# Kernel tuning notes

Hardware: AMD Instinct MI355X
Metric: run time of the kernel (lower is better)

The kernel has to match this reference:

```python
import jax, jax.numpy as jnp
import numpy as np

D_MODEL = 768
N_HEADS = 12
D_HEAD = 64
INIT_RANGE = 0.02
IGNORE = -100000.0


def setup_inputs() -> dict:
    key = jax.random.key(0)
    ks = jax.random.split(key, 5)
    x = jax.random.normal(ks[0], (2, 2048, D_MODEL), dtype=jnp.float32)
    W_Q = INIT_RANGE * jax.random.normal(ks[1], (N_HEADS, D_MODEL, D_HEAD), dtype=jnp.float32)
    W_K = INIT_RANGE * jax.random.normal(ks[2], (N_HEADS, D_MODEL, D_HEAD), dtype=jnp.float32)
    W_V = INIT_RANGE * jax.random.normal(ks[3], (N_HEADS, D_MODEL, D_HEAD), dtype=jnp.float32)
    W_O = INIT_RANGE * jax.random.normal(ks[4], (N_HEADS, D_HEAD, D_MODEL), dtype=jnp.float32)
    b_Q = jnp.zeros((N_HEADS, D_HEAD), dtype=jnp.float32)
    b_K = jnp.zeros((N_HEADS, D_HEAD), dtype=jnp.float32)
    b_V = jnp.zeros((N_HEADS, D_HEAD), dtype=jnp.float32)
    b_O = jnp.zeros((D_MODEL,), dtype=jnp.float32)
    return {"x": x, "W_Q": W_Q, "b_Q": b_Q, "W_K": W_K, "b_K": b_K,
            "W_V": W_V, "b_V": b_V, "W_O": W_O, "b_O": b_O}


def reference(x, W_Q, b_Q, W_K, b_K, W_V, b_V, W_O, b_O):
    # x: [b, s, m]; W_*: [h, m, d]
    Q = jnp.einsum('bsm,hmd->bshd', x, W_Q) + b_Q  # [b, s, h, d]
    K = jnp.einsum('bsm,hmd->bshd', x, W_K) + b_K
    V = jnp.einsum('bsm,hmd->bshd', x, W_V) + b_V
    scores = jnp.einsum('bqhd,bkhd->bhqk', Q, K) / jnp.sqrt(jnp.float32(D_HEAD))
    s = scores.shape[-1]
    causal = jnp.triu(jnp.ones((s, s), dtype=bool), k=1)  # True above diagonal
    scores = jnp.where(causal, jnp.float32(IGNORE), scores)
    pattern = jax.nn.softmax(scores, axis=-1)  # [b, h, q, k]
    Z = jnp.einsum('bhqk,bkhd->bqhd', pattern, V)
    out = jnp.einsum('bqhd,hdm->bqm', Z, W_O) + b_O
    return out
```

## Files before the change

kernel.cpp:

```cpp
#include <hip/hip_runtime.h>
#include <hip/hip_bf16.h>

#define BATCH 2
#define SLEN 2048
#define NH 12
#define DM 768
#define DH 64
#define ROWS (BATCH*SLEN)
#define NQKV (3*DM)
#define NCHUNK 51

typedef __attribute__((ext_vector_type(8))) short bf16x8;
typedef __attribute__((ext_vector_type(4))) float f32x4;
typedef unsigned short u16;
typedef unsigned int u32;
typedef __attribute__((ext_vector_type(4))) unsigned short u16x4;
typedef __attribute__((ext_vector_type(8))) unsigned short u16x8;

__device__ __forceinline__ u16 f2b(float f) {
    unsigned int u = __builtin_bit_cast(unsigned int, f);
    unsigned int r = (u + 0x7FFFu + ((u >> 16) & 1u)) >> 16;
    return (u16)r;
}
__device__ __forceinline__ float b2f(u16 v) {
    unsigned int u = ((unsigned int)v) << 16;
    return __builtin_bit_cast(float, u);
}

__device__ __forceinline__ void gload16(const u16* g, u16* l) {
    __builtin_amdgcn_global_load_lds(
        (const __attribute__((address_space(1))) unsigned int*)g,
        (__attribute__((address_space(3))) unsigned int*)l,
        16, 0, 0);
}


__global__ __launch_bounds__(256) void pack_x(const float* __restrict__ x, u16* __restrict__ xb) {
    int i = blockIdx.x * 256 + threadIdx.x;
    const float4* xv = (const float4*)x;
    float4 a = xv[i * 2], b = xv[i * 2 + 1];
    u16x8 o;
    o[0] = f2b(a.x); o[1] = f2b(a.y); o[2] = f2b(a.z); o[3] = f2b(a.w);
    o[4] = f2b(b.x); o[5] = f2b(b.y); o[6] = f2b(b.z); o[7] = f2b(b.w);
    *(u16x8*)(xb + (size_t)i * 8) = o;
}

__global__ __launch_bounds__(256) void pack_wqkv(const float* __restrict__ WQ, const float* __restrict__ WK,
                                                 const float* __restrict__ WV, u16* __restrict__ out) {
    __shared__ u16 L[64 * 72];
    int mt = blockIdx.x, h = blockIdx.y, sel = blockIdx.z;
    const float* W = sel == 0 ? WQ : (sel == 1 ? WK : WV);
    const float* src = W + ((size_t)h * DM + mt * 64) * DH;
    int t = threadIdx.x;
    for (int j = 0; j < 4; j++) {
        int i = t + 256 * j;
        int r = i >> 4, cf = i & 15;
        float4 v = ((const float4*)src)[i];
        u16x4 o; o[0] = f2b(v.x); o[1] = f2b(v.y); o[2] = f2b(v.z); o[3] = f2b(v.w);
        *(u16x4*)&L[r * 72 + cf * 4] = o;
    }
    __syncthreads();
    u16* orow = out + ((size_t)(sel * DM + h * DH)) * DM + mt * 64;
    for (int j = 0; j < 16; j++) {
        int e = t + 256 * j;
        int d = e >> 6, mm = e & 63;
        orow[(size_t)d * DM + mm] = L[mm * 72 + d];
    }
}

__global__ __launch_bounds__(256) void pack_wo(const float* __restrict__ WO, u16* __restrict__ out) {
    __shared__ u16 L[64 * 72];
    int bi = blockIdx.x, bj = blockIdx.y;
    int t = threadIdx.x;
    for (int j = 0; j < 4; j++) {
        int i = t + 256 * j;
        int r = i >> 4, cf = i & 15;
        float4 v = ((const float4*)(WO + (size_t)(bi * 64 + r) * DM + bj * 64))[cf];
        u16x4 o; o[0] = f2b(v.x); o[1] = f2b(v.y); o[2] = f2b(v.z); o[3] = f2b(v.w);
        *(u16x4*)&L[r * 72 + cf * 4] = o;
    }
    __syncthreads();
    for (int j = 0; j < 16; j++) {
        int e = t + 256 * j;
        int c = e >> 6, r = e & 63;
        out[(size_t)(bj * 64 + c) * DM + bi * 64 + r] = L[r * 72 + c];
    }
}


__global__ __launch_bounds__(256) void gemm_qkv(const u16* __restrict__ A, const u16* __restrict__ Bt,
                                                const float* __restrict__ bQ, const float* __restrict__ bK,
                                                const float* __restrict__ bV,
                                                u16* __restrict__ Qb, u16* __restrict__ Kb, u16* __restrict__ Vb) {
    __shared__ u16 Al[128 * 64];
    __shared__ u16 Bl[128 * 64];
    int t = threadIdx.x;
    int n0 = blockIdx.x * 128, m0 = blockIdx.y * 128;
    int lane = t & 63, w = t >> 6;
    int ln = lane & 15, qd = lane >> 4;
    int wr = (w & 1) * 64, wc = (w >> 1) * 64;
    int srow = lane >> 3, slot = lane & 7;
    f32x4 acc[4][4] = {};

    for (int kt = 0; kt < DM / 64; kt++) {
        __syncthreads();
        for (int j = 0; j < 4; j++) {
            int r = w * 32 + j * 8 + srow;
            int gc = slot ^ (r & 7);
            gload16(A + (size_t)(m0 + r) * DM + kt * 64 + gc * 8, &Al[(w * 32 + j * 8) * 64]);
            gload16(Bt + (size_t)(n0 + r) * DM + kt * 64 + gc * 8, &Bl[(w * 32 + j * 8) * 64]);
        }
        __syncthreads();
        for (int ks = 0; ks < 2; ks++) {
            int sl = ((ks * 4 + qd) ^ (ln & 7)) * 8;
            bf16x8 af[4], bfr[4];
            for (int rt = 0; rt < 4; rt++)
                af[rt] = *(const bf16x8*)&Al[(wr + rt * 16 + ln) * 64 + sl];
            for (int ct = 0; ct < 4; ct++)
                bfr[ct] = *(const bf16x8*)&Bl[(wc + ct * 16 + ln) * 64 + sl];
            for (int rt = 0; rt < 4; rt++)
                for (int ct = 0; ct < 4; ct++)
                    acc[rt][ct] = __builtin_amdgcn_mfma_f32_16x16x32_bf16(af[rt], bfr[ct], acc[rt][ct], 0, 0, 0);
        }
    }
    int sel = n0 / DM;
    if (sel == 2) {
        for (int ct = 0; ct < 4; ct++) {
            int col = n0 - 2 * DM + wc + ct * 16 + ln;
            int hh = col >> 6, dd = col & 63;
            float bv = bV[col];
            for (int rt = 0; rt < 4; rt++) {
                int row = m0 + wr + rt * 16 + qd * 4;
                int bb = row >> 11, ss = row & 2047;
                u16x4 pk;
                for (int r = 0; r < 4; r++) pk[r] = f2b(acc[rt][ct][r] + bv);
                *(u16x4*)&Vb[(((size_t)bb * NH + hh) * DH + dd) * SLEN + ss] = pk;
            }
        }
    } else {
        const float* bias = sel == 0 ? bQ : bK;
        u16* Out = sel == 0 ? Qb : Kb;
        const float qs = sel == 0 ? 0.125f * 1.44269504f : 1.0f;
        for (int ct = 0; ct < 4; ct++) {
            int col = n0 - sel * DM + wc + ct * 16 + ln;
            int hh = col >> 6, dd = col & 63;
            float bv = bias[col];
            for (int rt = 0; rt < 4; rt++) {
                int row = m0 + wr + rt * 16 + qd * 4;
                for (int r = 0; r < 4; r++) {
                    int rg = row + r;
                    int bb = rg >> 11, ss = rg & 2047;
                    Out[(((size_t)bb * NH + hh) * SLEN + ss) * DH + dd] = f2b((acc[rt][ct][r] + bv) * qs);
                }
            }
        }
    }
}


__device__ __forceinline__ void cid2qc(int cid, int& p, int& c, int& nc) {
    p = 0;
    int base = 0;
    while (true) {
        int n = p / 3 + 1;
        if (cid < base + n) { c = cid - base; nc = n; return; }
        base += n; p++;
    }
}

__global__ __launch_bounds__(256, 4) void attn(const u16* __restrict__ Qb, const u16* __restrict__ Kb,
                                               const u16* __restrict__ Vtg,
                                               u16* __restrict__ Po, float* __restrict__ Plv) {
    __shared__ u16 Kl[64 * 64];
    __shared__ u16 Vt[64 * 64];
    __shared__ u16 Pq[4 * 32 * 64];
    int cid = blockIdx.x, bh = blockIdx.y;
    int p, c, nc;
    cid2qc(cid, p, c, nc);
    int ntiles = 2 * p + 2;
    int kt0 = c * ntiles / nc, kt1 = (c + 1) * ntiles / nc;
    const u16* Qp = Qb + (size_t)bh * SLEN * DH;
    const u16* Kp = Kb + (size_t)bh * SLEN * DH;
    const u16* Vp = Vtg + (size_t)bh * SLEN * DH;
    int t = threadIdx.x, lane = t & 63, w = t >> 6;
    int ln = lane & 15, qd = lane >> 4;
    int srow = lane >> 3, slot = lane & 7;
    int qbA = p * 128 + w * 32, qbB = qbA + 16;

    bf16x8 qfA[2], qfB[2];
    for (int ks = 0; ks < 2; ks++) {
        qfA[ks] = *(const bf16x8*)(Qp + (size_t)(qbA + ln) * DH + ks * 32 + qd * 8);
        qfB[ks] = *(const bf16x8*)(Qp + (size_t)(qbB + ln) * DH + ks * 32 + qd * 8);
    }

    float lA = 0.f, lB = 0.f;
    f32x4 oA[4] = {}, oB[4] = {};

    u16* PwA = Pq + w * 32 * 64;
    u16* PwB = PwA + 16 * 64;

    for (int kt = kt0; kt < kt1; kt++) {
        int k0 = kt * 64;
        __syncthreads();
        for (int j = 0; j < 2; j++) {
            int r = w * 16 + j * 8 + srow;
            int gc = slot ^ (r & 7);
            gload16(Kp + (size_t)(k0 + r) * DH + gc * 8, &Kl[(w * 16 + j * 8) * 64]);
            gload16(Vp + (size_t)r * SLEN + k0 + gc * 8, &Vt[(w * 16 + j * 8) * 64]);
        }
        __syncthreads();

        f32x4 sfA[4] = {}, sfB[4] = {};
        for (int ks = 0; ks < 2; ks++) {
            int sl = ((ks * 4 + qd) ^ (ln & 7)) * 8;
            for (int ct = 0; ct < 4; ct++) {
                bf16x8 kf = *(const bf16x8*)&Kl[(ct * 16 + ln) * 64 + sl];
                sfA[ct] = __builtin_amdgcn_mfma_f32_16x16x32_bf16(kf, qfA[ks], sfA[ct], 0, 0, 0);
                sfB[ct] = __builtin_amdgcn_mfma_f32_16x16x32_bf16(kf, qfB[ks], sfB[ct], 0, 0, 0);
            }
        }

        if (kt >= (qbA >> 6)) {
            int qg = qbA + ln;
            for (int ct = 0; ct < 4; ct++)
                for (int r = 0; r < 4; r++) {
                    int kg = k0 + ct * 16 + qd * 4 + r;
                    if (kg > qg) sfA[ct][r] = -1e30f;
                }
        }
        if (kt >= (qbB >> 6)) {
            int qg = qbB + ln;
            for (int ct = 0; ct < 4; ct++)
                for (int r = 0; r < 4; r++) {
                    int kg = k0 + ct * 16 + qd * 4 + r;
                    if (kg > qg) sfB[ct][r] = -1e30f;
                }
        }

        float sA = 0.f, sB = 0.f;
        for (int ct = 0; ct < 4; ct++) {
            u32 ea[4], eb[4];
            for (int r = 0; r < 4; r++) {
                float eA = exp2f(sfA[ct][r]);
                float eB = exp2f(sfB[ct][r]);
                ea[r] = __builtin_bit_cast(u32, eA);
                eb[r] = __builtin_bit_cast(u32, eB);
                sA += __builtin_bit_cast(float, ea[r] & 0xFFFF0000u);
                sB += __builtin_bit_cast(float, eb[r] & 0xFFFF0000u);
            }
            uint2 pkA, pkB;
            pkA.x = __builtin_amdgcn_perm(ea[1], ea[0], 0x07060302u);
            pkA.y = __builtin_amdgcn_perm(ea[3], ea[2], 0x07060302u);
            pkB.x = __builtin_amdgcn_perm(eb[1], eb[0], 0x07060302u);
            pkB.y = __builtin_amdgcn_perm(eb[3], eb[2], 0x07060302u);
            int off = (((ct * 2 + (qd >> 1)) ^ (ln & 7)) * 8) + (qd & 1) * 4;
            *(uint2*)&PwA[ln * 64 + off] = pkA;
            *(uint2*)&PwB[ln * 64 + off] = pkB;
        }
        lA += sA; lB += sB;

        for (int ks = 0; ks < 2; ks++) {
            int sl = ((ks * 4 + qd) ^ (ln & 7)) * 8;
            bf16x8 pfA = *(const bf16x8*)&PwA[ln * 64 + sl];
            bf16x8 pfB = *(const bf16x8*)&PwB[ln * 64 + sl];
            for (int dt = 0; dt < 4; dt++) {
                bf16x8 vf = *(const bf16x8*)&Vt[(dt * 16 + ln) * 64 + sl];
                oA[dt] = __builtin_amdgcn_mfma_f32_16x16x32_bf16(vf, pfA, oA[dt], 0, 0, 0);
                oB[dt] = __builtin_amdgcn_mfma_f32_16x16x32_bf16(vf, pfB, oB[dt], 0, 0, 0);
            }
        }
    }

    lA += __shfl_xor(lA, 16, 64);
    lA += __shfl_xor(lA, 32, 64);
    lB += __shfl_xor(lB, 16, 64);
    lB += __shfl_xor(lB, 32, 64);

    size_t pid = (size_t)bh * NCHUNK + cid;
    u16* op = Po + pid * 8192;
    for (int dt = 0; dt < 4; dt++) {
        u16x4 ovA, ovB;
        for (int r = 0; r < 4; r++) { ovA[r] = f2b(oA[dt][r]); ovB[r] = f2b(oB[dt][r]); }
        *(u16x4*)&op[(w * 32 + ln) * 64 + dt * 16 + qd * 4] = ovA;
        *(u16x4*)&op[(w * 32 + 16 + ln) * 64 + dt * 16 + qd * 4] = ovB;
    }
    if (qd == 0) {
        Plv[pid * 128 + w * 32 + ln] = lA;
        Plv[pid * 128 + w * 32 + 16 + ln] = lB;
    }
}


__global__ __launch_bounds__(256) void combine(const u16* __restrict__ Po, const float* __restrict__ Plv,
                                               u16* __restrict__ Zb) {
    int p = blockIdx.x, bh = blockIdx.y;
    int b = bh / NH, h = bh % NH;
    int g = p / 3, i = p % 3;
    int nc = g + 1;
    int base = 3 * (g * (g + 1) / 2) + i * (g + 1);
    int t = threadIdx.x;
    int q = t >> 1, dseg = (t & 1) * 32;

    float acc[32] = {};
    float lsum = 0.f;
    for (int cc = 0; cc < nc; cc++) {
        size_t pid = (size_t)bh * NCHUNK + base + cc;
        lsum += Plv[pid * 128 + q];
        const u16* op = Po + pid * 8192 + q * 64 + dseg;
        for (int j = 0; j < 4; j++) {
            u16x8 v = *(const u16x8*)(op + j * 8);
            for (int e = 0; e < 8; e++)
                acc[j * 8 + e] += b2f(v[e]);
        }
    }
    float inv = 1.0f / lsum;
    u16* Zp = Zb + ((size_t)b * SLEN + p * 128 + q) * DM + h * DH + dseg;
    for (int j = 0; j < 4; j++) {
        u16x8 ov;
        for (int e = 0; e < 8; e++) ov[e] = f2b(acc[j * 8 + e] * inv);
        *(u16x8*)(Zp + j * 8) = ov;
    }
}


__global__ __launch_bounds__(256) void gemm_proj(const u16* __restrict__ A, const u16* __restrict__ Bt,
                                                 const float* __restrict__ bO, float* __restrict__ out) {
    __shared__ u16 Al[64 * 64];
    __shared__ u16 Bl[96 * 64];
    int t = threadIdx.x;
    int n0 = blockIdx.x * 96, m0 = blockIdx.y * 64;
    int lane = t & 63, w = t >> 6;
    int ln = lane & 15, qd = lane >> 4;
    int wr = (w & 1) * 32, wc = (w >> 1) * 48;
    int srow = lane >> 3, slot = lane & 7;
    f32x4 acc[2][3] = {};

    for (int kt = 0; kt < DM / 64; kt++) {
        __syncthreads();
        for (int j = 0; j < 2; j++) {
            int r = w * 16 + j * 8 + srow;
            int gc = slot ^ (r & 7);
            gload16(A + (size_t)(m0 + r) * DM + kt * 64 + gc * 8, &Al[(w * 16 + j * 8) * 64]);
        }
        for (int j = 0; j < 3; j++) {
            int r = w * 24 + j * 8 + srow;
            int gc = slot ^ (r & 7);
            gload16(Bt + (size_t)(n0 + r) * DM + kt * 64 + gc * 8, &Bl[(w * 24 + j * 8) * 64]);
        }
        __syncthreads();
        for (int ks = 0; ks < 2; ks++) {
            int sl = ((ks * 4 + qd) ^ (ln & 7)) * 8;
            bf16x8 af[2], bfr[3];
            for (int rt = 0; rt < 2; rt++)
                af[rt] = *(const bf16x8*)&Al[(wr + rt * 16 + ln) * 64 + sl];
            for (int ct = 0; ct < 3; ct++)
                bfr[ct] = *(const bf16x8*)&Bl[(wc + ct * 16 + ln) * 64 + sl];
            for (int rt = 0; rt < 2; rt++)
                for (int ct = 0; ct < 3; ct++)
                    acc[rt][ct] = __builtin_amdgcn_mfma_f32_16x16x32_bf16(af[rt], bfr[ct], acc[rt][ct], 0, 0, 0);
        }
    }
    for (int ct = 0; ct < 3; ct++) {
        int col = n0 + wc + ct * 16 + ln;
        float bv = bO[col];
        for (int rt = 0; rt < 2; rt++) {
            int row = m0 + wr + rt * 16 + qd * 4;
            for (int r = 0; r < 4; r++)
                out[(size_t)(row + r) * DM + col] = acc[rt][ct][r] + bv;
        }
    }
}


extern "C" void kernel_launch(void* const* d_in, const int* in_sizes, int n_in,
                              void* d_out, int out_size, void* d_ws, size_t ws_size,
                              hipStream_t stream) {
    const float* x  = (const float*)d_in[0];
    const float* WQ = (const float*)d_in[1];
    const float* bQ = (const float*)d_in[2];
    const float* WK = (const float*)d_in[3];
    const float* bK = (const float*)d_in[4];
    const float* WV = (const float*)d_in[5];
    const float* bV = (const float*)d_in[6];
    const float* WO = (const float*)d_in[7];
    const float* bO = (const float*)d_in[8];
    float* out = (float*)d_out;

    u16* xb   = (u16*)d_ws;
    u16* wqkv = xb + (size_t)ROWS * DM;
    u16* wo   = wqkv + (size_t)NQKV * DM;
    u16* Qb   = wo + (size_t)DM * DM;
    size_t hsz = (size_t)BATCH * NH * SLEN * DH;
    u16* Kb   = Qb + hsz;
    u16* Vb   = Kb + hsz;
    u16* Zb   = Vb + hsz;
    u16* Po   = Zb + (size_t)ROWS * DM;
    float* Pl = (float*)(Po + (size_t)BATCH * NH * NCHUNK * 8192);

    pack_x<<<ROWS * DM / 2048, 256, 0, stream>>>(x, xb);
    pack_wqkv<<<dim3(12, 12, 3), 256, 0, stream>>>(WQ, WK, WV, wqkv);
    pack_wo<<<dim3(12, 12), 256, 0, stream>>>(WO, wo);
    gemm_qkv<<<dim3(NQKV / 128, ROWS / 128), 256, 0, stream>>>(xb, wqkv, bQ, bK, bV, Qb, Kb, Vb);
    attn<<<dim3(NCHUNK, BATCH * NH), 256, 0, stream>>>(Qb, Kb, Vb, Po, Pl);
    combine<<<dim3(SLEN / 128, BATCH * NH), 256, 0, stream>>>(Po, Pl, Zb);
    gemm_proj<<<dim3(DM / 96, ROWS / 64), 256, 0, stream>>>(Zb, wo, bO, out);
}
```

Measured before the change: 182.8 us.

## Double-buffer K/V tiles in attention and remap grid to a 1D interleaved order

The attention kernel now keeps two LDS buffers for the K and V tiles. It issues the load of the next tile right after the barrier, so the global-to-LDS copy overlaps the current tile's QK and PV MFMAs, and each iteration needs one barrier instead of two. The per-wave P scratch shrinks to one 16x64 tile that the A and B query halves use in turn, which offsets part of the extra LDS from double buffering. The launch becomes a 1D grid that interleaves batch-head indices across consecutive blocks, likely to spread K/V reuse across XCDs and caches. Total LDS per block rises, which could limit occupancy, and reusing one P buffer serializes the two softmax/PV halves.

New measurement: 202.8 us. 10.9% more time.

```diff
diff --git a/kernel.cpp b/kernel.cpp
--- a/kernel.cpp
+++ b/kernel.cpp
@@ -171,10 +171,13 @@
 __global__ __launch_bounds__(256, 4) void attn(const u16* __restrict__ Qb, const u16* __restrict__ Kb,
                                                const u16* __restrict__ Vtg,
                                                u16* __restrict__ Po, float* __restrict__ Plv) {
-    __shared__ u16 Kl[64 * 64];
-    __shared__ u16 Vt[64 * 64];
-    __shared__ u16 Pq[4 * 32 * 64];
-    int cid = blockIdx.x, bh = blockIdx.y;
+    __shared__ u16 Kl[2][64 * 64];
+    __shared__ u16 Vt[2][64 * 64];
+    __shared__ u16 Pq[4][16 * 64];
+    int blk = blockIdx.x;
+    int j24 = blk % 24;
+    int cid = blk / 24;
+    int bh = (j24 & 7) * 3 + (j24 >> 3);
     int p, c, nc;
     cid2qc(cid, p, c, nc);
     int ntiles = 2 * p + 2;
@@ -195,26 +198,57 @@
 
     float lA = 0.f, lB = 0.f;
     f32x4 oA[4] = {}, oB[4] = {};
-
-    u16* PwA = Pq + w * 32 * 64;
-    u16* PwB = PwA + 16 * 64;
-
-    for (int kt = kt0; kt < kt1; kt++) {
+    u16* Pw = Pq[w];
+    int cur = 0;
+
+    auto stage = [&](int kt, int buf) {
         int k0 = kt * 64;
-        __syncthreads();
         for (int j = 0; j < 2; j++) {
             int r = w * 16 + j * 8 + srow;
             int gc = slot ^ (r & 7);
-            gload16(Kp + (size_t)(k0 + r) * DH + gc * 8, &Kl[(w * 16 + j * 8) * 64]);
-            gload16(Vp + (size_t)r * SLEN + k0 + gc * 8, &Vt[(w * 16 + j * 8) * 64]);
-        }
+            gload16(Kp + (size_t)(k0 + r) * DH + gc * 8, &Kl[buf][(w * 16 + j * 8) * 64]);
+            gload16(Vp + (size_t)r * SLEN + k0 + gc * 8, &Vt[buf][(w * 16 + j * 8) * 64]);
+        }
+    };
+
+    auto frag = [&](f32x4 (&sf)[4], float& l, f32x4 (&o)[4]) {
+        float s = 0.f;
+        for (int ct = 0; ct < 4; ct++) {
+            u32 e4[4];
+            for (int r = 0; r < 4; r++) {
+                float e = exp2f(sf[ct][r]);
+                e4[r] = __builtin_bit_cast(u32, e);
+                s += __builtin_bit_cast(float, e4[r] & 0xFFFF0000u);
+            }
+            uint2 pk;
+            pk.x = __builtin_amdgcn_perm(e4[1], e4[0], 0x07060302u);
+            pk.y = __builtin_amdgcn_perm(e4[3], e4[2], 0x07060302u);
+            int off = (((ct * 2 + (qd >> 1)) ^ (ln & 7)) * 8) + (qd & 1) * 4;
+            *(uint2*)&Pw[ln * 64 + off] = pk;
+        }
+        l += s;
+        for (int ks = 0; ks < 2; ks++) {
+            int sl = ((ks * 4 + qd) ^ (ln & 7)) * 8;
+            bf16x8 pf = *(const bf16x8*)&Pw[ln * 64 + sl];
+            for (int dt = 0; dt < 4; dt++) {
+                bf16x8 vf = *(const bf16x8*)&Vt[cur][(dt * 16 + ln) * 64 + sl];
+                o[dt] = __builtin_amdgcn_mfma_f32_16x16x32_bf16(vf, pf, o[dt], 0, 0, 0);
+            }
+        }
+    };
+
+    stage(kt0, 0);
+    for (int kt = kt0; kt < kt1; kt++) {
+        cur = (kt - kt0) & 1;
+        int k0 = kt * 64;
         __syncthreads();
+        if (kt + 1 < kt1) stage(kt + 1, cur ^ 1);
 
         f32x4 sfA[4] = {}, sfB[4] = {};
         for (int ks = 0; ks < 2; ks++) {
             int sl = ((ks * 4 + qd) ^ (ln & 7)) * 8;
             for (int ct = 0; ct < 4; ct++) {
-                bf16x8 kf = *(const bf16x8*)&Kl[(ct * 16 + ln) * 64 + sl];
+                bf16x8 kf = *(const bf16x8*)&Kl[cur][(ct * 16 + ln) * 64 + sl];
                 sfA[ct] = __builtin_amdgcn_mfma_f32_16x16x32_bf16(kf, qfA[ks], sfA[ct], 0, 0, 0);
                 sfB[ct] = __builtin_amdgcn_mfma_f32_16x16x32_bf16(kf, qfB[ks], sfB[ct], 0, 0, 0);
             }
@@ -237,38 +271,8 @@
                 }
         }
 
-        float sA = 0.f, sB = 0.f;
-        for (int ct = 0; ct < 4; ct++) {
-            u32 ea[4], eb[4];
-            for (int r = 0; r < 4; r++) {
-                float eA = exp2f(sfA[ct][r]);
-                float eB = exp2f(sfB[ct][r]);
-                ea[r] = __builtin_bit_cast(u32, eA);
-                eb[r] = __builtin_bit_cast(u32, eB);
-                sA += __builtin_bit_cast(float, ea[r] & 0xFFFF0000u);
-                sB += __builtin_bit_cast(float, eb[r] & 0xFFFF0000u);
-            }
-            uint2 pkA, pkB;
-            pkA.x = __builtin_amdgcn_perm(ea[1], ea[0], 0x07060302u);
-            pkA.y = __builtin_amdgcn_perm(ea[3], ea[2], 0x07060302u);
-            pkB.x = __builtin_amdgcn_perm(eb[1], eb[0], 0x07060302u);
-            pkB.y = __builtin_amdgcn_perm(eb[3], eb[2], 0x07060302u);
-            int off = (((ct * 2 + (qd >> 1)) ^ (ln & 7)) * 8) + (qd & 1) * 4;
-            *(uint2*)&PwA[ln * 64 + off] = pkA;
-            *(uint2*)&PwB[ln * 64 + off] = pkB;
-        }
-        lA += sA; lB += sB;
-
-        for (int ks = 0; ks < 2; ks++) {
-            int sl = ((ks * 4 + qd) ^ (ln & 7)) * 8;
-            bf16x8 pfA = *(const bf16x8*)&PwA[ln * 64 + sl];
-            bf16x8 pfB = *(const bf16x8*)&PwB[ln * 64 + sl];
-            for (int dt = 0; dt < 4; dt++) {
-                bf16x8 vf = *(const bf16x8*)&Vt[(dt * 16 + ln) * 64 + sl];
-                oA[dt] = __builtin_amdgcn_mfma_f32_16x16x32_bf16(vf, pfA, oA[dt], 0, 0, 0);
-                oB[dt] = __builtin_amdgcn_mfma_f32_16x16x32_bf16(vf, pfB, oB[dt], 0, 0, 0);
-            }
-        }
+        frag(sfA, lA, oA);
+        frag(sfB, lB, oB);
     }
 
     lA += __shfl_xor(lA, 16, 64);
@@ -401,7 +405,7 @@
     pack_wqkv<<<dim3(12, 12, 3), 256, 0, stream>>>(WQ, WK, WV, wqkv);
     pack_wo<<<dim3(12, 12), 256, 0, stream>>>(WO, wo);
     gemm_qkv<<<dim3(NQKV / 128, ROWS / 128), 256, 0, stream>>>(xb, wqkv, bQ, bK, bV, Qb, Kb, Vb);
-    attn<<<dim3(NCHUNK, BATCH * NH), 256, 0, stream>>>(Qb, Kb, Vb, Po, Pl);
+    attn<<<dim3(NCHUNK * 24), 256, 0, stream>>>(Qb, Kb, Vb, Po, Pl);
     combine<<<dim3(SLEN / 128, BATCH * NH), 256, 0, stream>>>(Po, Pl, Zb);
     gemm_proj<<<dim3(DM / 96, ROWS / 64), 256, 0, stream>>>(Zb, wo, bO, out);
 }
```
